# Kernel tuning notes

Hardware: AMD Instinct MI355X
Metric: run time of the kernel (lower is better)

## Reference

```python
import jax, jax.numpy as jnp
import numpy as np

TAU_U = 1.0
TAU_L = 0.05
EPS = 1e-12  # torch F.normalize eps


def setup_inputs() -> dict:
    key = jax.random.key(0)
    ks = jax.random.split(key, 8)
    N, D, B = 100000, 128, 8192
    x1 = jax.random.normal(ks[0], (N, D), dtype=jnp.float32)
    x2 = jax.random.normal(ks[1], (N, D), dtype=jnp.float32)
    x1_index = jax.random.randint(ks[2], (B,), 0, N, dtype=jnp.int64 if jax.config.jax_enable_x64 else jnp.int32)
    x2_index = jax.random.randint(ks[3], (B,), 0, N, dtype=jnp.int64 if jax.config.jax_enable_x64 else jnp.int32)
    # Linear params (torch Linear default init: U(-1/sqrt(fan_in), 1/sqrt(fan_in)))
    lim1 = 1.0 / np.sqrt(D)
    W1 = jax.random.uniform(ks[4], (D, D), minval=-lim1, maxval=lim1, dtype=jnp.float32)
    b1 = jax.random.uniform(ks[5], (D,), minval=-lim1, maxval=lim1, dtype=jnp.float32)
    W2 = jax.random.uniform(ks[6], (1, D), minval=-lim1, maxval=lim1, dtype=jnp.float32)
    b2 = jax.random.uniform(ks[7], (1,), minval=-lim1, maxval=lim1, dtype=jnp.float32)
    return {"x1": x1, "x2": x2, "x1_index": x1_index, "x2_index": x2_index,
            "W1": W1, "b1": b1, "W2": W2, "b2": b2}


def _l2norm(x):
    # matches torch F.normalize(dim=1) for 2-D input
    n = jnp.sqrt(jnp.sum(x * x, axis=-1, keepdims=True))
    return x / jnp.maximum(n, EPS)


def reference(x1, x2, x1_index, x2_index, W1, b1, W2, b2):
    x1_feat = _l2norm(x1[x1_index])          # [B, D]
    x2_feat = _l2norm(x2[x2_index])          # [B, D]

    h = x1_feat * x2_feat                    # [B, D]
    h = h @ W1.T + b1                        # lin1
    h = jnp.where(h >= 0, h, 0.2 * h)        # leaky_relu(0.2)
    s = jax.nn.sigmoid(h @ W2.T + b2)        # [B, 1]
    ssl_temp = (TAU_U - TAU_L) * (1.0 - s) + TAU_L   # [B, 1]

    pos = jnp.sum(x1_feat * x2_feat, axis=-1)         # [B]
    # NOTE: [B] / [B,1] broadcasts to [B,B] exactly like torch
    pos_rating = jnp.exp(pos / ssl_temp)              # [B, B]

    tot = x1_feat @ x2_feat.T                          # [B, B]
    tot_rating = jnp.sum(jnp.exp(tot / ssl_temp), axis=1)  # [B]

    ssl_temp_avg = jnp.mean(ssl_temp)
    return (pos_rating, tot_rating, ssl_temp_avg)
```

## Files before the change

### kernel.cpp

```cpp
#include <hip/hip_runtime.h>
#include <stdint.h>

typedef __bf16 bf16x8 __attribute__((ext_vector_type(8)));
typedef float f32x4 __attribute__((ext_vector_type(4)));
typedef __attribute__((address_space(3))) uint32_t as3u32;
typedef const __attribute__((address_space(1))) uint32_t as1u32;

#define B_TOT 8192
#define DD 128
#define OUT_TOT 67108864UL
#define OUT_AVG 67117056UL

__device__ inline unsigned short f2bf(float x){
  union { float f; uint32_t u; } v; v.f = x;
  return (unsigned short)((v.u + 0x7fffu + ((v.u >> 16) & 1u)) >> 16);
}

__global__ __launch_bounds__(256) void k_feat(const float* __restrict__ x1,
    const float* __restrict__ x2, const int* __restrict__ i1a, const int* __restrict__ i2a,
    unsigned short* __restrict__ f1b, unsigned short* __restrict__ f2b,
    unsigned short* __restrict__ hb, float* __restrict__ posw, float* __restrict__ out){
  int tid = threadIdx.x;
  int gid = blockIdx.x * 256 + tid;
  if (gid <= 8192) out[OUT_TOT + gid] = 0.f;
  int w = tid >> 6, l = tid & 63;
  int b = blockIdx.x * 4 + w;
  const float2* r1 = (const float2*)(x1 + (size_t)i1a[b] * DD);
  const float2* r2 = (const float2*)(x2 + (size_t)i2a[b] * DD);
  float2 v1 = r1[l], v2 = r2[l];
  float s1 = v1.x * v1.x + v1.y * v1.y;
  float s2 = v2.x * v2.x + v2.y * v2.y;
  #pragma unroll
  for (int o = 32; o; o >>= 1){ s1 += __shfl_xor(s1, o); s2 += __shfl_xor(s2, o); }
  float inv1 = 1.f / fmaxf(sqrtf(s1), 1e-12f);
  float inv2 = 1.f / fmaxf(sqrtf(s2), 1e-12f);
  float f1x = v1.x * inv1, f1y = v1.y * inv1;
  float f2x = v2.x * inv2, f2y = v2.y * inv2;
  float hx = f1x * f2x, hy = f1y * f2y;
  float ps = hx + hy;
  #pragma unroll
  for (int o = 32; o; o >>= 1) ps += __shfl_xor(ps, o);
  unsigned int u1 = (unsigned int)f2bf(f1x) | ((unsigned int)f2bf(f1y) << 16);
  unsigned int u2 = (unsigned int)f2bf(f2x) | ((unsigned int)f2bf(f2y) << 16);
  unsigned int uh = (unsigned int)f2bf(hx)  | ((unsigned int)f2bf(hy)  << 16);
  ((unsigned int*)f1b)[b * 64 + l] = u1;
  ((unsigned int*)f2b)[b * 64 + l] = u2;
  ((unsigned int*)hb)[b * 64 + l]  = uh;
  if (l == 0) posw[b] = ps;
}

__device__ inline void stage_tile(const unsigned short* g, unsigned short* s){
  int tid = threadIdx.x;
  #pragma unroll
  for (int it = 0; it < 8; ++it){
    int c = tid + it * 256;
    int row = c >> 4, cc = c & 15;
    int src = (row << 4) + (cc ^ (row & 7));
    __builtin_amdgcn_global_load_lds((as1u32*)(g + src * 8),
                                     (as3u32*)(s + c * 8), 16, 0, 0);
  }
}
__device__ inline void stage_tile64(const unsigned short* g, unsigned short* s){
  int tid = threadIdx.x;
  #pragma unroll
  for (int it = 0; it < 4; ++it){
    int c = tid + it * 256;
    int row = c >> 4, cc = c & 15;
    int src = (row << 4) + (cc ^ (row & 7));
    __builtin_amdgcn_global_load_lds((as1u32*)(g + src * 8),
                                     (as3u32*)(s + c * 8), 16, 0, 0);
  }
}

__device__ inline void mfma_tile(const unsigned short* As, const unsigned short* Bs,
                                 f32x4 acc[4][4]){
  int tid = threadIdx.x;
  int w = tid >> 6, l = tid & 63;
  int wr = (w >> 1) * 64, wc = (w & 1) * 64;
  int lo = l & 15, hi = l >> 4;
  f32x4 zero = {0.f, 0.f, 0.f, 0.f};
  #pragma unroll
  for (int m = 0; m < 4; ++m)
    #pragma unroll
    for (int n = 0; n < 4; ++n) acc[m][n] = zero;
  #pragma unroll
  for (int kk = 0; kk < 4; ++kk){
    bf16x8 af[4], bfv[4];
    #pragma unroll
    for (int m = 0; m < 4; ++m){
      int row = wr + m * 16 + lo;
      af[m] = *(const bf16x8*)(As + row * 128 + ((kk * 4 + hi) ^ (row & 7)) * 8);
    }
    #pragma unroll
    for (int n = 0; n < 4; ++n){
      int row = wc + n * 16 + lo;
      bfv[n] = *(const bf16x8*)(Bs + row * 128 + ((kk * 4 + hi) ^ (row & 7)) * 8);
    }
    #pragma unroll
    for (int m = 0; m < 4; ++m)
      #pragma unroll
      for (int n = 0; n < 4; ++n)
        acc[m][n] = __builtin_amdgcn_mfma_f32_16x16x32_bf16(af[m], bfv[n], acc[m][n], 0, 0, 0);
  }
}

__global__ __launch_bounds__(256) void k_lin(const unsigned short* __restrict__ hb,
    const float* __restrict__ W1, const float* __restrict__ b1,
    const float* __restrict__ W2, const float* __restrict__ b2,
    float* __restrict__ rTw, float* __restrict__ out){
  __shared__ __align__(16) unsigned short As[16384];
  __shared__ __align__(16) unsigned short Bs[16384];
  __shared__ float zpart[2][128];
  __shared__ float s4[4];
  int i0 = blockIdx.x * 128;
  int tid = threadIdx.x;
  stage_tile(hb + (size_t)i0 * 128, As);
  #pragma unroll
  for (int it = 0; it < 8; ++it){
    int c = tid + it * 256;
    int row = c >> 4, cc = c & 15;
    int src = (row << 4) + (cc ^ (row & 7));
    const float4* g4 = (const float4*)(W1 + src * 8);
    float4 a = g4[0], b = g4[1];
    unsigned short t8[8];
    t8[0] = f2bf(a.x); t8[1] = f2bf(a.y); t8[2] = f2bf(a.z); t8[3] = f2bf(a.w);
    t8[4] = f2bf(b.x); t8[5] = f2bf(b.y); t8[6] = f2bf(b.z); t8[7] = f2bf(b.w);
    *(uint4*)(Bs + c * 8) = *(uint4*)t8;
  }
  asm volatile("s_waitcnt vmcnt(0)" ::: "memory");
  __syncthreads();
  f32x4 acc[4][4];
  mfma_tile(As, Bs, acc);
  int w = tid >> 6, l = tid & 63;
  int wrb = (w >> 1) * 64, wcb = (w & 1) * 64, lo = l & 15, hi = l >> 4;
  float w2v[4], b1v[4];
  #pragma unroll
  for (int n = 0; n < 4; ++n){ int col = wcb + n * 16 + lo; w2v[n] = W2[col]; b1v[n] = b1[col]; }
  #pragma unroll
  for (int m = 0; m < 4; ++m){
    #pragma unroll
    for (int q = 0; q < 4; ++q){
      float p = 0.f;
      #pragma unroll
      for (int n = 0; n < 4; ++n){
        float hv = acc[m][n][q] + b1v[n];
        hv = hv >= 0.f ? hv : 0.2f * hv;
        p += hv * w2v[n];
      }
      p += __shfl_xor(p, 1); p += __shfl_xor(p, 2);
      p += __shfl_xor(p, 4); p += __shfl_xor(p, 8);
      if (lo == 0) zpart[w & 1][wrb + m * 16 + hi * 4 + q] = p;
    }
  }
  __syncthreads();
  float Tloc = 0.f;
  if (tid < 128){
    float z = zpart[0][tid] + zpart[1][tid] + b2[0];
    float s = 1.f / (1.f + __expf(-z));
    float T = 0.95f * (1.f - s) + 0.05f;
    rTw[i0 + tid] = 1.f / T;
    Tloc = T;
  }
  float v = Tloc;
  #pragma unroll
  for (int o = 32; o; o >>= 1) v += __shfl_xor(v, o);
  if ((tid & 63) == 0) s4[tid >> 6] = v;
  __syncthreads();
  if (tid == 0) atomicAdd(out + OUT_AVG, (s4[0] + s4[1] + s4[2] + s4[3]) * (1.0f / 8192.0f));
}

__global__ __launch_bounds__(256, 2) void k_tot(const unsigned short* __restrict__ f1b,
    const unsigned short* __restrict__ f2b, const float* __restrict__ rTw,
    float* __restrict__ out){
  __shared__ __align__(16) unsigned short Abuf[16384];
  __shared__ __align__(16) unsigned short Bbuf0[8192];
  __shared__ __align__(16) unsigned short Bbuf1[8192];
  __shared__ __align__(16) float rS[128];
  int s = (blockIdx.x & 7) * 64 + (blockIdx.x >> 3);
  int rt = s & 63, ctg = s >> 6;
  int tid = threadIdx.x, w = tid >> 6, l = tid & 63;
  int wr = (w >> 1) * 64, wc = (w & 1) * 32;
  int lo = l & 15, hi = l >> 4;
  const unsigned short* Bg = f2b + (size_t)(ctg * 1024) * 128;
  stage_tile(f1b + (size_t)rt * 16384, Abuf);
  if (tid < 32)
    __builtin_amdgcn_global_load_lds((as1u32*)(rTw + rt * 128 + tid * 4),
                                     (as3u32*)(rS + tid * 4), 16, 0, 0);
  stage_tile64(Bg, Bbuf0);
  stage_tile64(Bg + 64 * 128, Bbuf1);
  asm volatile("s_waitcnt vmcnt(0)" ::: "memory");
  __builtin_amdgcn_s_barrier();
  bf16x8 af[4][4];
  #pragma unroll
  for (int kk = 0; kk < 4; ++kk)
    #pragma unroll
    for (int m = 0; m < 4; ++m){
      int row = wr + m * 16 + lo;
      af[kk][m] = *(const bf16x8*)(Abuf + row * 128 + ((kk * 4 + hi) ^ (row & 7)) * 8);
    }
  float pacc[4][4] = {{0.f,0.f,0.f,0.f},{0.f,0.f,0.f,0.f},{0.f,0.f,0.f,0.f},{0.f,0.f,0.f,0.f}};
  unsigned short* ba = Bbuf0;
  unsigned short* bb = Bbuf1;
  #pragma unroll 1
  for (int i = 0; i < 16; ++i){
    if (i < 15) asm volatile("s_waitcnt vmcnt(4)" ::: "memory");
    else        asm volatile("s_waitcnt vmcnt(0)" ::: "memory");
    __builtin_amdgcn_s_barrier();
    f32x4 acc[4][2];
    f32x4 zero = {0.f,0.f,0.f,0.f};
    #pragma unroll
    for (int m = 0; m < 4; ++m){ acc[m][0] = zero; acc[m][1] = zero; }
    #pragma unroll
    for (int kk = 0; kk < 4; ++kk){
      bf16x8 bfv[2];
      #pragma unroll
      for (int n = 0; n < 2; ++n){
        int row = wc + n * 16 + lo;
        bfv[n] = *(const bf16x8*)(ba + row * 128 + ((kk * 4 + hi) ^ (row & 7)) * 8);
      }
      #pragma unroll
      for (int m = 0; m < 4; ++m){
        acc[m][0] = __builtin_amdgcn_mfma_f32_16x16x32_bf16(af[kk][m], bfv[0], acc[m][0], 0, 0, 0);
        acc[m][1] = __builtin_amdgcn_mfma_f32_16x16x32_bf16(af[kk][m], bfv[1], acc[m][1], 0, 0, 0);
      }
    }
    asm volatile("s_waitcnt lgkmcnt(0)" ::: "memory");
    __builtin_amdgcn_s_barrier();
    if (i < 14) stage_tile64(Bg + (size_t)(i + 2) * 64 * 128, ba);
    #pragma unroll
    for (int m = 0; m < 4; ++m)
      #pragma unroll
      for (int q = 0; q < 4; ++q){
        float r = rS[wr + m * 16 + hi * 4 + q];
        pacc[m][q] += __expf(acc[m][0][q] * r) + __expf(acc[m][1][q] * r);
      }
    unsigned short* t = ba; ba = bb; bb = t;
  }
  #pragma unroll
  for (int m = 0; m < 4; ++m)
    #pragma unroll
    for (int q = 0; q < 4; ++q){
      float p = pacc[m][q];
      p += __shfl_xor(p, 1); p += __shfl_xor(p, 2);
      p += __shfl_xor(p, 4); p += __shfl_xor(p, 8);
      if (lo == 0) atomicAdd(out + OUT_TOT + rt * 128 + wr + m * 16 + hi * 4 + q, p);
    }
}

__global__ __launch_bounds__(256) void k_pr(const float* __restrict__ posw,
    const float* __restrict__ rTw, float* __restrict__ out){
  int tid = threadIdx.x;
  int r0 = blockIdx.x * 4;
  f32x4 p[8];
  #pragma unroll
  for (int c = 0; c < 8; ++c) p[c] = *(const f32x4*)(posw + (c * 256 + tid) * 4);
  float4 rr4 = *(const float4*)(rTw + r0);
  float rr[4] = {rr4.x, rr4.y, rr4.z, rr4.w};
  #pragma unroll
  for (int r = 0; r < 4; ++r){
    float* ob = out + (size_t)(r0 + r) * B_TOT;
    #pragma unroll
    for (int c = 0; c < 8; ++c){
      f32x4 e;
      e.x = __expf(p[c].x * rr[r]); e.y = __expf(p[c].y * rr[r]);
      e.z = __expf(p[c].z * rr[r]); e.w = __expf(p[c].w * rr[r]);
      *(f32x4*)(ob + (c * 256 + tid) * 4) = e;
    }
  }
}

extern "C" void kernel_launch(void* const* d_in, const int* in_sizes, int n_in,
                              void* d_out, int out_size, void* d_ws, size_t ws_size,
                              hipStream_t stream){
  const float* x1 = (const float*)d_in[0];
  const float* x2 = (const float*)d_in[1];
  const int*   i1 = (const int*)d_in[2];
  const int*   i2 = (const int*)d_in[3];
  const float* W1 = (const float*)d_in[4];
  const float* b1 = (const float*)d_in[5];
  const float* W2 = (const float*)d_in[6];
  const float* b2 = (const float*)d_in[7];
  float* out = (float*)d_out;
  char* ws = (char*)d_ws;
  unsigned short* hb   = (unsigned short*)(ws);
  unsigned short* f1b  = (unsigned short*)(ws + 2097152);
  unsigned short* f2b  = (unsigned short*)(ws + 4194304);
  float* posw  = (float*)(ws + 6291456);
  float* rTw   = (float*)(ws + 6324224);

  hipLaunchKernelGGL(k_feat, dim3(2048), dim3(256), 0, stream, x1, x2, i1, i2, f1b, f2b, hb, posw, out);
  hipLaunchKernelGGL(k_lin,  dim3(64),   dim3(256), 0, stream, hb, W1, b1, W2, b2, rTw, out);
  hipLaunchKernelGGL(k_tot,  dim3(512),  dim3(256), 0, stream, f1b, f2b, rTw, out);
  hipLaunchKernelGGL(k_pr,   dim3(2048), dim3(256), 0, stream, posw, rTw, out);
}
```

Before: 87.68 us.

## Fuse gather/normalize with lin1 MLP in fp32 and drop atomic temperature mean

Merges the feature kernel and the lin1/leaky-relu/lin2/sigmoid kernel into one 512-thread kernel. Each block stages all of W1 into LDS as fp32 and computes the per-row MLP with scalar FMAs, which removes the bf16 hb round trip and one launch. The temperature mean is now built from per-block partials that the first k_pr block reduces, replacing the atomicAdd. The cost is that every one of 1024 blocks reloads the 64KB W1 into LDS, and the MLP now runs on plain FMAs instead of MFMA.

```diff
diff --git a/kernel.cpp b/kernel.cpp
--- a/kernel.cpp
+++ b/kernel.cpp
@@ -16,15 +16,29 @@
   return (unsigned short)((v.u + 0x7fffu + ((v.u >> 16) & 1u)) >> 16);
 }
 
-__global__ __launch_bounds__(256) void k_feat(const float* __restrict__ x1,
+__global__ __launch_bounds__(512) void k_fl(const float* __restrict__ x1,
     const float* __restrict__ x2, const int* __restrict__ i1a, const int* __restrict__ i2a,
+    const float* __restrict__ W1, const float* __restrict__ b1,
+    const float* __restrict__ W2, const float* __restrict__ b2,
     unsigned short* __restrict__ f1b, unsigned short* __restrict__ f2b,
-    unsigned short* __restrict__ hb, float* __restrict__ posw, float* __restrict__ out){
-  int tid = threadIdx.x;
-  int gid = blockIdx.x * 256 + tid;
-  if (gid <= 8192) out[OUT_TOT + gid] = 0.f;
+    float* __restrict__ posw, float* __restrict__ rTw, float* __restrict__ Tpart,
+    float* __restrict__ out){
+  __shared__ __align__(16) float W1S[16384];
+  __shared__ __align__(16) float hS[8][128];
+  __shared__ float TS[8];
+  int tid = threadIdx.x;
+  int gid = blockIdx.x * 512 + tid;
+  if (gid < 8192) out[OUT_TOT + gid] = 0.f;
+  #pragma unroll
+  for (int it = 0; it < 8; ++it){
+    int c = tid + it * 512;
+    int j = c >> 5, u = c & 31;
+    int src = (j << 5) + (u ^ (j & 31));
+    __builtin_amdgcn_global_load_lds((as1u32*)(W1 + src * 4),
+                                     (as3u32*)(W1S + c * 4), 16, 0, 0);
+  }
   int w = tid >> 6, l = tid & 63;
-  int b = blockIdx.x * 4 + w;
+  int b = blockIdx.x * 8 + w;
   const float2* r1 = (const float2*)(x1 + (size_t)i1a[b] * DD);
   const float2* r2 = (const float2*)(x2 + (size_t)i2a[b] * DD);
   float2 v1 = r1[l], v2 = r2[l];
@@ -42,11 +56,39 @@
   for (int o = 32; o; o >>= 1) ps += __shfl_xor(ps, o);
   unsigned int u1 = (unsigned int)f2bf(f1x) | ((unsigned int)f2bf(f1y) << 16);
   unsigned int u2 = (unsigned int)f2bf(f2x) | ((unsigned int)f2bf(f2y) << 16);
-  unsigned int uh = (unsigned int)f2bf(hx)  | ((unsigned int)f2bf(hy)  << 16);
   ((unsigned int*)f1b)[b * 64 + l] = u1;
   ((unsigned int*)f2b)[b * 64 + l] = u2;
-  ((unsigned int*)hb)[b * 64 + l]  = uh;
   if (l == 0) posw[b] = ps;
+  *(float2*)&hS[w][2 * l] = make_float2(hx, hy);
+  asm volatile("s_waitcnt vmcnt(0)" ::: "memory");
+  __syncthreads();
+  int j1 = l, j2 = l + 64, lm = l & 31;
+  float z1 = 0.f, z2 = 0.f;
+  #pragma unroll 8
+  for (int u = 0; u < 32; ++u){
+    f32x4 hq = *(const f32x4*)&hS[w][u * 4];
+    f32x4 wa = *(const f32x4*)(W1S + j1 * 128 + ((u ^ lm) << 2));
+    f32x4 wb = *(const f32x4*)(W1S + j2 * 128 + ((u ^ lm) << 2));
+    z1 += hq.x * wa.x + hq.y * wa.y + hq.z * wa.z + hq.w * wa.w;
+    z2 += hq.x * wb.x + hq.y * wb.y + hq.z * wb.z + hq.w * wb.w;
+  }
+  z1 += b1[j1]; z2 += b1[j2];
+  z1 = z1 >= 0.f ? z1 : 0.2f * z1;
+  z2 = z2 >= 0.f ? z2 : 0.2f * z2;
+  float p = z1 * W2[j1] + z2 * W2[j2];
+  #pragma unroll
+  for (int o = 32; o; o >>= 1) p += __shfl_xor(p, o);
+  float zz = p + b2[0];
+  float sg = 1.f / (1.f + __expf(-zz));
+  float T = 0.95f * (1.f - sg) + 0.05f;
+  if (l == 0){ rTw[b] = 1.f / T; TS[w] = T; }
+  __syncthreads();
+  if (tid == 0){
+    float t = 0.f;
+    #pragma unroll
+    for (int q = 0; q < 8; ++q) t += TS[q];
+    Tpart[blockIdx.x] = t;
+  }
 }
 
 __device__ inline void stage_tile(const unsigned short* g, unsigned short* s){
@@ -70,103 +112,6 @@
     __builtin_amdgcn_global_load_lds((as1u32*)(g + src * 8),
                                      (as3u32*)(s + c * 8), 16, 0, 0);
   }
-}
-
-__device__ inline void mfma_tile(const unsigned short* As, const unsigned short* Bs,
-                                 f32x4 acc[4][4]){
-  int tid = threadIdx.x;
-  int w = tid >> 6, l = tid & 63;
-  int wr = (w >> 1) * 64, wc = (w & 1) * 64;
-  int lo = l & 15, hi = l >> 4;
-  f32x4 zero = {0.f, 0.f, 0.f, 0.f};
-  #pragma unroll
-  for (int m = 0; m < 4; ++m)
-    #pragma unroll
-    for (int n = 0; n < 4; ++n) acc[m][n] = zero;
-  #pragma unroll
-  for (int kk = 0; kk < 4; ++kk){
-    bf16x8 af[4], bfv[4];
-    #pragma unroll
-    for (int m = 0; m < 4; ++m){
-      int row = wr + m * 16 + lo;
-      af[m] = *(const bf16x8*)(As + row * 128 + ((kk * 4 + hi) ^ (row & 7)) * 8);
-    }
-    #pragma unroll
-    for (int n = 0; n < 4; ++n){
-      int row = wc + n * 16 + lo;
-      bfv[n] = *(const bf16x8*)(Bs + row * 128 + ((kk * 4 + hi) ^ (row & 7)) * 8);
-    }
-    #pragma unroll
-    for (int m = 0; m < 4; ++m)
-      #pragma unroll
-      for (int n = 0; n < 4; ++n)
-        acc[m][n] = __builtin_amdgcn_mfma_f32_16x16x32_bf16(af[m], bfv[n], acc[m][n], 0, 0, 0);
-  }
-}
-
-__global__ __launch_bounds__(256) void k_lin(const unsigned short* __restrict__ hb,
-    const float* __restrict__ W1, const float* __restrict__ b1,
-    const float* __restrict__ W2, const float* __restrict__ b2,
-    float* __restrict__ rTw, float* __restrict__ out){
-  __shared__ __align__(16) unsigned short As[16384];
-  __shared__ __align__(16) unsigned short Bs[16384];
-  __shared__ float zpart[2][128];
-  __shared__ float s4[4];
-  int i0 = blockIdx.x * 128;
-  int tid = threadIdx.x;
-  stage_tile(hb + (size_t)i0 * 128, As);
-  #pragma unroll
-  for (int it = 0; it < 8; ++it){
-    int c = tid + it * 256;
-    int row = c >> 4, cc = c & 15;
-    int src = (row << 4) + (cc ^ (row & 7));
-    const float4* g4 = (const float4*)(W1 + src * 8);
-    float4 a = g4[0], b = g4[1];
-    unsigned short t8[8];
-    t8[0] = f2bf(a.x); t8[1] = f2bf(a.y); t8[2] = f2bf(a.z); t8[3] = f2bf(a.w);
-    t8[4] = f2bf(b.x); t8[5] = f2bf(b.y); t8[6] = f2bf(b.z); t8[7] = f2bf(b.w);
-    *(uint4*)(Bs + c * 8) = *(uint4*)t8;
-  }
-  asm volatile("s_waitcnt vmcnt(0)" ::: "memory");
-  __syncthreads();
-  f32x4 acc[4][4];
-  mfma_tile(As, Bs, acc);
-  int w = tid >> 6, l = tid & 63;
-  int wrb = (w >> 1) * 64, wcb = (w & 1) * 64, lo = l & 15, hi = l >> 4;
-  float w2v[4], b1v[4];
-  #pragma unroll
-  for (int n = 0; n < 4; ++n){ int col = wcb + n * 16 + lo; w2v[n] = W2[col]; b1v[n] = b1[col]; }
-  #pragma unroll
-  for (int m = 0; m < 4; ++m){
-    #pragma unroll
-    for (int q = 0; q < 4; ++q){
-      float p = 0.f;
-      #pragma unroll
-      for (int n = 0; n < 4; ++n){
-        float hv = acc[m][n][q] + b1v[n];
-        hv = hv >= 0.f ? hv : 0.2f * hv;
-        p += hv * w2v[n];
-      }
-      p += __shfl_xor(p, 1); p += __shfl_xor(p, 2);
-      p += __shfl_xor(p, 4); p += __shfl_xor(p, 8);
-      if (lo == 0) zpart[w & 1][wrb + m * 16 + hi * 4 + q] = p;
-    }
-  }
-  __syncthreads();
-  float Tloc = 0.f;
-  if (tid < 128){
-    float z = zpart[0][tid] + zpart[1][tid] + b2[0];
-    float s = 1.f / (1.f + __expf(-z));
-    float T = 0.95f * (1.f - s) + 0.05f;
-    rTw[i0 + tid] = 1.f / T;
-    Tloc = T;
-  }
-  float v = Tloc;
-  #pragma unroll
-  for (int o = 32; o; o >>= 1) v += __shfl_xor(v, o);
-  if ((tid & 63) == 0) s4[tid >> 6] = v;
-  __syncthreads();
-  if (tid == 0) atomicAdd(out + OUT_AVG, (s4[0] + s4[1] + s4[2] + s4[3]) * (1.0f / 8192.0f));
 }
 
 __global__ __launch_bounds__(256, 2) void k_tot(const unsigned short* __restrict__ f1b,
@@ -248,8 +193,18 @@
 }
 
 __global__ __launch_bounds__(256) void k_pr(const float* __restrict__ posw,
-    const float* __restrict__ rTw, float* __restrict__ out){
-  int tid = threadIdx.x;
+    const float* __restrict__ rTw, const float* __restrict__ Tpart,
+    float* __restrict__ out){
+  int tid = threadIdx.x;
+  if (blockIdx.x == 0){
+    float t = Tpart[tid * 4] + Tpart[tid * 4 + 1] + Tpart[tid * 4 + 2] + Tpart[tid * 4 + 3];
+    #pragma unroll
+    for (int o = 32; o; o >>= 1) t += __shfl_xor(t, o);
+    __shared__ float tsum[4];
+    if ((tid & 63) == 0) tsum[tid >> 6] = t;
+    __syncthreads();
+    if (tid == 0) out[OUT_AVG] = (tsum[0] + tsum[1] + tsum[2] + tsum[3]) * (1.f / 8192.f);
+  }
   int r0 = blockIdx.x * 4;
   f32x4 p[8];
   #pragma unroll
@@ -282,14 +237,14 @@
   const float* b2 = (const float*)d_in[7];
   float* out = (float*)d_out;
   char* ws = (char*)d_ws;
-  unsigned short* hb   = (unsigned short*)(ws);
   unsigned short* f1b  = (unsigned short*)(ws + 2097152);
   unsigned short* f2b  = (unsigned short*)(ws + 4194304);
   float* posw  = (float*)(ws + 6291456);
   float* rTw   = (float*)(ws + 6324224);
-
-  hipLaunchKernelGGL(k_feat, dim3(2048), dim3(256), 0, stream, x1, x2, i1, i2, f1b, f2b, hb, posw, out);
-  hipLaunchKernelGGL(k_lin,  dim3(64),   dim3(256), 0, stream, hb, W1, b1, W2, b2, rTw, out);
-  hipLaunchKernelGGL(k_tot,  dim3(512),  dim3(256), 0, stream, f1b, f2b, rTw, out);
-  hipLaunchKernelGGL(k_pr,   dim3(2048), dim3(256), 0, stream, posw, rTw, out);
-}
+  float* Tpart = (float*)(ws + 6356992);
+
+  hipLaunchKernelGGL(k_fl,  dim3(1024), dim3(512), 0, stream,
+                     x1, x2, i1, i2, W1, b1, W2, b2, f1b, f2b, posw, rTw, Tpart, out);
+  hipLaunchKernelGGL(k_tot, dim3(512),  dim3(256), 0, stream, f1b, f2b, rTw, out);
+  hipLaunchKernelGGL(k_pr,  dim3(2048), dim3(256), 0, stream, posw, rTw, Tpart, out);
+}
```

New measurement: 90.25 us. 2.9% more time.
